# Performance work log

Hardware: AMD Instinct MI355X
Metric: run time of the kernel (lower is better)

## Reference

```python
import jax, jax.numpy as jnp
from jax import lax
import numpy as np

B, C, H, W = 8, 128, 112, 112
G, K, OC = 4, 3, 128
DN = ('NCHW', 'OIHW', 'NCHW')


def setup_inputs() -> dict:
    key = jax.random.key(0)
    k1, k2, k3, k4, k5 = jax.random.split(key, 5)
    x = jax.random.normal(k1, (B, C, H, W), dtype=jnp.float32)
    # kernel_gen: grouped conv, out = K*K*G channels, in/group = C//G
    w_kg = jax.random.normal(k2, (K * K * G, C // G, K, K), dtype=jnp.float32) * 0.05
    b_kg = jax.random.normal(k3, (K * K * G,), dtype=jnp.float32) * 0.05
    # pointwise_conv: grouped 1x1 conv, out = OC, in/group = C//G
    w_pw = jax.random.normal(k4, (OC, C // G, 1, 1), dtype=jnp.float32) * 0.05
    b_pw = jax.random.normal(k5, (OC,), dtype=jnp.float32) * 0.05
    return {"x": x, "w_kg": w_kg, "b_kg": b_kg, "w_pw": w_pw, "b_pw": b_pw}


def reference(x, w_kg, b_kg, w_pw, b_pw):
    b, c, h, w = x.shape
    # dynamic per-pixel kernels: [B, G*K*K, H, W] -> [B, G, K*K, H, W]
    kernel = lax.conv_general_dilated(
        x, w_kg, (1, 1), ((K // 2, K // 2), (K // 2, K // 2)),
        feature_group_count=G, dimension_numbers=DN)
    kernel = kernel + b_kg[None, :, None, None]
    kernel = kernel.reshape(b, G, K * K, h, w)
    # unfold (stride=1, pad=K//2): channel-major, kernel-offset row-major (matches F.unfold)
    p = K // 2
    xp = jnp.pad(x, ((0, 0), (0, 0), (p, p), (p, p)))
    patches = jnp.stack(
        [xp[:, :, i:i + h, j:j + w] for i in range(K) for j in range(K)],
        axis=2)  # [B, C, K*K, H, W]
    patches = patches.reshape(b, G, c // G, K * K, h, w)
    # per-pixel multiply-reduce over kernel taps
    out = (patches * kernel[:, :, None]).sum(axis=3).reshape(b, c, h, w)
    # grouped 1x1 pointwise conv
    out = lax.conv_general_dilated(
        out, w_pw, (1, 1), 'VALID', feature_group_count=G, dimension_numbers=DN)
    return out + b_pw[None, :, None, None]
```

## Files before the change

### kernel.cpp

```cpp
#include <hip/hip_runtime.h>
#include <hip/hip_bf16.h>

typedef __attribute__((ext_vector_type(8))) short short8;
typedef __attribute__((ext_vector_type(4))) float f32x4;
typedef __attribute__((ext_vector_type(4))) unsigned int u32x4;

#define GG 4
#define CC 128
#define HH 112
#define WW 112
#define HWSZ (HH * WW)
#define TH 16
#define TW 16
#define HALO 18
#define NPIX (HALO * HALO)
#define XSTR 32
#define HP 114
#define SLICE_PIX (HP * HP)
#define SLICE_ELE (SLICE_PIX * 32)
#define WK_ELEMS (4 * 9 * 16 * 32)
#define WP_ELEMS (4 * 2 * 16 * 32)
#define W_TOTAL (WK_ELEMS + WP_ELEMS)
#define XT_OFF 32768
#define XT_ELEMS (32 * SLICE_ELE)
#define WS_NEED ((size_t)(XT_OFF + XT_ELEMS) * 2)


__device__ __forceinline__ void reorder_one(int idx,
    const float* __restrict__ w_kg, const float* __restrict__ w_pw,
    unsigned short* __restrict__ ws)
{
    if (idx < WK_ELEMS) {
        int c = idx & 31, t = (idx >> 5) & 15, r = idx >> 9;
        int u = r % 9, g = r / 9;
        float v = (t < 9) ? w_kg[((g * 9 + t) * 32 + c) * 9 + u] : 0.0f;
        ws[idx] = __builtin_bit_cast(unsigned short, __float2bfloat16(v));
    } else if (idx < W_TOTAL) {
        int j = idx - WK_ELEMS;
        int c = j & 31, o = (j >> 5) & 15, mt = (j >> 9) & 1, g = j >> 10;
        float v = w_pw[(g * 32 + mt * 16 + o) * 32 + c];
        ws[idx] = __builtin_bit_cast(unsigned short, __float2bfloat16(v));
    }
}

__global__ __launch_bounds__(256)
void reorder_weights(const float* __restrict__ w_kg, const float* __restrict__ w_pw,
                     unsigned short* __restrict__ ws)
{
    reorder_one(blockIdx.x * 256 + threadIdx.x, w_kg, w_pw, ws);
}

__global__ __launch_bounds__(256, 4)
void transpose_x(const float* __restrict__ x,
                 const float* __restrict__ w_kg, const float* __restrict__ w_pw,
                 unsigned short* __restrict__ ws)
{
    __shared__ unsigned int xsT[16 * 452];
    const int hc = blockIdx.x;
    const int g = blockIdx.y, b = blockIdx.z;
    const int tid = threadIdx.x;
    const int slice = b * GG + g;
    unsigned short* xt = ws + XT_OFF;

    if (hc == 28) {
        #pragma unroll
        for (int k = 0; k < 3; ++k) {
            int off = k * 256 + tid;
            if (off < 704)
                reorder_one(slice * 704 + off, w_kg, w_pw, ws);
        }
        return;
    }
    if (hc == 29) {
        unsigned short* xts = xt + (size_t)slice * SLICE_ELE;
        short8 z = {0, 0, 0, 0, 0, 0, 0, 0};
        #pragma unroll
        for (int k = 0; k < 2; ++k) {
            int i = tid + 256 * k;
            if (i < 452) {
                int pix;
                if (i < 114)      pix = i;
                else if (i < 228) pix = 113 * HP + (i - 114);
                else if (i < 340) pix = (i - 228 + 1) * HP;
                else              pix = (i - 340 + 1) * HP + 113;
                unsigned short* d = xts + (size_t)pix * 32;
                *(short8*)(d)      = z;
                *(short8*)(d + 8)  = z;
                *(short8*)(d + 16) = z;
                *(short8*)(d + 24) = z;
            }
        }
        return;
    }

    const float* xg = x + (size_t)(b * CC + g * 32) * HWSZ + hc * 4 * WW;

    unsigned short* xsT16 = (unsigned short*)xsT;
    #pragma unroll
    for (int k = 0; k < 14; ++k) {
        int t = tid + 256 * k;
        int c = (t * 37450) >> 22;
        int p4 = t - c * 112;
        float4 v = *(const float4*)(xg + (size_t)c * HWSZ + 4 * p4);
        int base = ((c >> 1) * 452 + 4 * p4) * 2 + (c & 1);
        xsT16[base + 0] = __builtin_bit_cast(unsigned short, __float2bfloat16(v.x));
        xsT16[base + 2] = __builtin_bit_cast(unsigned short, __float2bfloat16(v.y));
        xsT16[base + 4] = __builtin_bit_cast(unsigned short, __float2bfloat16(v.z));
        xsT16[base + 6] = __builtin_bit_cast(unsigned short, __float2bfloat16(v.w));
    }
    __syncthreads();

    unsigned short* xts = xt + (size_t)slice * SLICE_ELE;
    #pragma unroll
    for (int k = 0; k < 7; ++k) {
        int t = tid + 256 * k;
        int p = t >> 2, kb = t & 3;
        int row = p / 112;
        int col = p - 112 * row;
        unsigned r[4];
        #pragma unroll
        for (int j = 0; j < 4; ++j)
            r[j] = xsT[(4 * kb + j) * 452 + p];
        size_t pix = (size_t)(hc * 4 + row + 1) * HP + (col + 1);
        *(u32x4*)(xts + pix * 32 + kb * 8) = (u32x4){r[0], r[1], r[2], r[3]};
    }
}

struct Frags {
    short8 afrag[9];
    short8 wpfrag[2];
    float bkv[4];
    float bpv[8];
};

__device__ __forceinline__ void load_frags(Frags& f,
    const unsigned short* __restrict__ wsw,
    const float* __restrict__ b_kg, const float* __restrict__ b_pw,
    int g, int tid)
{
    const int lane = tid & 63;
    const int px   = lane & 15;
    const int kb   = lane >> 4;

    #pragma unroll
    for (int u = 0; u < 9; ++u)
        f.afrag[u] = *(const short8*)(wsw + (((g * 9 + u) * 16 + px) * 32 + kb * 8));
    #pragma unroll
    for (int mt = 0; mt < 2; ++mt)
        f.wpfrag[mt] = *(const short8*)(wsw + WK_ELEMS + (((g * 2 + mt) * 16 + px) * 32 + kb * 8));

    const float* bk = b_kg + g * 9;
    const float* bp = b_pw + g * 32;
    #pragma unroll
    for (int e = 0; e < 4; ++e) {
        int t = 4 * kb + e;
        f.bkv[e] = bk[t < 9 ? t : 0];
    }
    #pragma unroll
    for (int mt = 0; mt < 2; ++mt)
        #pragma unroll
        for (int e = 0; e < 4; ++e)
            f.bpv[mt * 4 + e] = bp[mt * 16 + 4 * kb + e];
}

__device__ __forceinline__ void compute_tile(const Frags& f,
    float* __restrict__ out, unsigned short* xs, float* kvl,
    int g, int b, int h0, int w0, int tid)
{
    const int lane = tid & 63;
    const int wid  = tid >> 6;
    const int px   = lane & 15;
    const int kb   = lane >> 4;

    float* kvp = &kvl[(wid * 16 + px) * 9];
    const size_t obase = ((size_t)(b * CC + g * 32) * HH + h0) * WW + w0 + px;

    #pragma unroll 1
    for (int r = 0; r < 4; ++r) {
        const int py = wid * 4 + r;

        short8 bfrag[9];
        #pragma unroll
        for (int u = 0; u < 9; ++u) {
            int q = (py + u / 3) * HALO + (px + u % 3);
            bfrag[u] = *(const short8*)&xs[q * XSTR + kb * 8];
        }

        f32x4 kv = {0.f, 0.f, 0.f, 0.f};
        #pragma unroll
        for (int u = 0; u < 9; ++u)
            kv = __builtin_amdgcn_mfma_f32_16x16x32_bf16(f.afrag[u], bfrag[u], kv, 0, 0, 0);

        if (kb < 2) {
            #pragma unroll
            for (int i = 0; i < 4; ++i)
                kvp[4 * kb + i] = kv[i] + f.bkv[i];
        } else if (kb == 2) {
            kvp[8] = kv[0] + f.bkv[0];
        }
        float kvv[9];
        #pragma unroll
        for (int t = 0; t < 9; ++t) kvv[t] = kvp[t];

        float m[8] = {0.f, 0.f, 0.f, 0.f, 0.f, 0.f, 0.f, 0.f};
        #pragma unroll
        for (int u = 0; u < 9; ++u) {
            u32x4 bu = __builtin_bit_cast(u32x4, bfrag[u]);
            #pragma unroll
            for (int w = 0; w < 4; ++w) {
                unsigned d = bu[w];
                float lo = __builtin_bit_cast(float, d << 16);
                float hi = __builtin_bit_cast(float, d & 0xffff0000u);
                m[2 * w]     = fmaf(lo, kvv[u], m[2 * w]);
                m[2 * w + 1] = fmaf(hi, kvv[u], m[2 * w + 1]);
            }
        }

        unsigned pk[4];
        #pragma unroll
        for (int w = 0; w < 4; ++w) {
            unsigned slo = __builtin_bit_cast(unsigned short, __float2bfloat16(m[2 * w]));
            unsigned shi = __builtin_bit_cast(unsigned short, __float2bfloat16(m[2 * w + 1]));
            pk[w] = slo | (shi << 16);
        }
        short8 mfrag = __builtin_bit_cast(short8, (u32x4){pk[0], pk[1], pk[2], pk[3]});

        f32x4 zero = {0.f, 0.f, 0.f, 0.f};
        f32x4 o0 = __builtin_amdgcn_mfma_f32_16x16x32_bf16(f.wpfrag[0], mfrag, zero, 0, 0, 0);
        f32x4 o1 = __builtin_amdgcn_mfma_f32_16x16x32_bf16(f.wpfrag[1], mfrag, zero, 0, 0, 0);

        #pragma unroll
        for (int e = 0; e < 4; ++e) {
            int o = 4 * kb + e;
            out[obase + (size_t)o * HWSZ + (size_t)py * WW] = o0[e] + f.bpv[e];
            out[obase + (size_t)(o + 16) * HWSZ + (size_t)py * WW] = o1[e] + f.bpv[4 + e];
        }
    }
}

__global__ __launch_bounds__(256, 4)
void invol_mfma(const unsigned short* __restrict__ ws_all,
                const float* __restrict__ b_kg, const float* __restrict__ b_pw,
                float* __restrict__ out)
{
    __shared__ unsigned short xs[NPIX * XSTR];
    __shared__ float kvl[4 * 16 * 9];

    const int tile  = blockIdx.x;
    const int tileh = tile / 7;
    const int tilew = tile - tileh * 7;
    const int g = blockIdx.y;
    const int b = blockIdx.z;
    const int h0 = tileh * TH;
    const int w0 = tilew * TW;
    const int tid = threadIdx.x;

    {
        const unsigned short* xti = ws_all + XT_OFF + (size_t)(b * GG + g) * SLICE_ELE;
        #pragma unroll
        for (int k = 0; k < 6; ++k) {
            int t = tid + 256 * k;
            if (t < 1296) {
                int q = t >> 2, kb2 = t & 3;
                int r = (q * 57) >> 10;
                int col = q - 18 * r;
                const unsigned short* src =
                    xti + ((size_t)((h0 + r) * HP + (w0 + col)) * 32 + kb2 * 8);
                __builtin_amdgcn_global_load_lds(src, &xs[t * 8], 16, 0, 0);
            }
        }
    }

    Frags f;
    load_frags(f, ws_all, b_kg, b_pw, g, tid);

    __syncthreads();

    compute_tile(f, out, xs, kvl, g, b, h0, w0, tid);
}

__global__ __launch_bounds__(256, 4)
void invol_mfma_fb(const float* __restrict__ x,
                   const float* __restrict__ b_kg, const float* __restrict__ b_pw,
                   const unsigned short* __restrict__ ws, float* __restrict__ out)
{
    __shared__ unsigned short xs[NPIX * XSTR];
    __shared__ float kvl[4 * 16 * 9];

    const int tile  = blockIdx.x;
    const int tileh = tile / 7;
    const int tilew = tile - tileh * 7;
    const int g = blockIdx.y;
    const int b = blockIdx.z;
    const int h0 = tileh * TH;
    const int w0 = tilew * TW;
    const int tid = threadIdx.x;

    Frags f;
    load_frags(f, ws, b_kg, b_pw, g, tid);

    {
        const float* xg = x + (size_t)(b * CC + g * 32) * HWSZ;
        int c = 0, q = tid;
        #pragma unroll
        for (int batch = 0; batch < 3; ++batch) {
            const int bn = (batch == 2) ? 13 : 14;
            float v[14];
            int pki[14];
            #pragma unroll
            for (int it = 0; it < bn; ++it) {
                const int itg = batch * 14 + it;
                const bool valid = (itg < 40) || (tid < 128);
                int r   = (q * 57) >> 10;
                int col = q - 18 * r;
                int gh = h0 - 1 + r;
                int gw = w0 - 1 + col;
                bool ok = valid && ((unsigned)gh < (unsigned)HH) && ((unsigned)gw < (unsigned)WW);
                int ghc = min(max(gh, 0), HH - 1);
                int gwc = min(max(gw, 0), WW - 1);
                int cc  = min(c, 31);
                float t = xg[(size_t)cc * HWSZ + ghc * WW + gwc];
                v[it]   = ok ? t : 0.0f;
                pki[it] = (c < 32) ? (q * XSTR + c) : 0;
                q += 256; if (q >= NPIX) { q -= NPIX; ++c; }
            }
            #pragma unroll
            for (int it = 0; it < bn; ++it) {
                unsigned short val = __builtin_bit_cast(unsigned short, __float2bfloat16(v[it]));
                if (pki[it] || it == 0) xs[pki[it]] = val;
            }
        }
    }
    __syncthreads();

    compute_tile(f, out, xs, kvl, g, b, h0, w0, tid);
}

extern "C" void kernel_launch(void* const* d_in, const int* in_sizes, int n_in,
                              void* d_out, int out_size, void* d_ws, size_t ws_size,
                              hipStream_t stream)
{
    const float* x    = (const float*)d_in[0];
    const float* w_kg = (const float*)d_in[1];
    const float* b_kg = (const float*)d_in[2];
    const float* w_pw = (const float*)d_in[3];
    const float* b_pw = (const float*)d_in[4];
    float* out = (float*)d_out;
    unsigned short* ws = (unsigned short*)d_ws;

    if (ws_size >= WS_NEED) {
        hipLaunchKernelGGL(transpose_x, dim3(30, GG, 8), dim3(256), 0, stream,
                           x, w_kg, w_pw, ws);
        hipLaunchKernelGGL(invol_mfma, dim3(49, GG, 8), dim3(256), 0, stream,
                           ws, b_kg, b_pw, out);
    } else {
        int pre_blocks = (W_TOTAL + 255) / 256;
        hipLaunchKernelGGL(reorder_weights, dim3(pre_blocks), dim3(256), 0, stream,
                           w_kg, w_pw, ws);
        hipLaunchKernelGGL(invol_mfma_fb, dim3(49, GG, 8), dim3(256), 0, stream,
                           x, b_kg, b_pw, ws, out);
    }
}
```

Measured before the change: 36.00 us.

## Give each wave a private halo slice in LDS and drop block barrier

Each wave now loads its own 6-row halo strip (4 output rows plus 2 halo rows) into a private LDS region. That replaces the shared 18x18 tile and the block-wide __syncthreads with a per-wave vmcnt wait. The goal is to remove inter-wave synchronisation so waves start computing as soon as their own data arrives. In exchange, halo rows are loaded redundantly (24 rows instead of 18) and the LDS footprint grows, which could reduce occupancy. The per-wave kvl use already appears wave-private.

```diff
diff --git a/kernel.cpp b/kernel.cpp
--- a/kernel.cpp
+++ b/kernel.cpp
@@ -15,6 +15,8 @@
 #define HALO 18
 #define NPIX (HALO * HALO)
 #define XSTR 32
+#define WCH 432
+#define WUS (WCH * 8)
 #define HP 114
 #define SLICE_PIX (HP * HP)
 #define SLICE_ELE (SLICE_PIX * 32)
@@ -163,6 +165,7 @@
             f.bpv[mt * 4 + e] = bp[mt * 16 + 4 * kb + e];
 }
 
+template<bool WL>
 __device__ __forceinline__ void compute_tile(const Frags& f,
     float* __restrict__ out, unsigned short* xs, float* kvl,
     int g, int b, int h0, int w0, int tid)
@@ -172,6 +175,7 @@
     const int px   = lane & 15;
     const int kb   = lane >> 4;
 
+    const unsigned short* xw = WL ? (xs + wid * WUS) : xs;
     float* kvp = &kvl[(wid * 16 + px) * 9];
     const size_t obase = ((size_t)(b * CC + g * 32) * HH + h0) * WW + w0 + px;
 
@@ -182,8 +186,9 @@
         short8 bfrag[9];
         #pragma unroll
         for (int u = 0; u < 9; ++u) {
-            int q = (py + u / 3) * HALO + (px + u % 3);
-            bfrag[u] = *(const short8*)&xs[q * XSTR + kb * 8];
+            int prow = WL ? (r + u / 3) : (py + u / 3);
+            int pix  = prow * HALO + (px + u % 3);
+            bfrag[u] = *(const short8*)&xw[pix * XSTR + kb * 8];
         }
 
         f32x4 kv = {0.f, 0.f, 0.f, 0.f};
@@ -243,7 +248,7 @@
                 const float* __restrict__ b_kg, const float* __restrict__ b_pw,
                 float* __restrict__ out)
 {
-    __shared__ unsigned short xs[NPIX * XSTR];
+    __shared__ unsigned short xs[4 * WUS];
     __shared__ float kvl[4 * 16 * 9];
 
     const int tile  = blockIdx.x;
@@ -254,19 +259,23 @@
     const int h0 = tileh * TH;
     const int w0 = tilew * TW;
     const int tid = threadIdx.x;
+    const int lane = tid & 63;
+    const int wid  = tid >> 6;
 
     {
         const unsigned short* xti = ws_all + XT_OFF + (size_t)(b * GG + g) * SLICE_ELE;
-        #pragma unroll
-        for (int k = 0; k < 6; ++k) {
-            int t = tid + 256 * k;
-            if (t < 1296) {
-                int q = t >> 2, kb2 = t & 3;
-                int r = (q * 57) >> 10;
-                int col = q - 18 * r;
+        const int R0 = wid * 4;
+        unsigned short* xw = xs + wid * WUS;
+        #pragma unroll
+        for (int k = 0; k < 7; ++k) {
+            int t = lane + 64 * k;
+            if (k < 6 || t < WCH) {
+                int lr  = (t * 57) >> 12;
+                int rem = t - 72 * lr;
+                int col = rem >> 2, kb2 = rem & 3;
                 const unsigned short* src =
-                    xti + ((size_t)((h0 + r) * HP + (w0 + col)) * 32 + kb2 * 8);
-                __builtin_amdgcn_global_load_lds(src, &xs[t * 8], 16, 0, 0);
+                    xti + ((size_t)((h0 + R0 + lr) * HP + (w0 + col)) * 32 + kb2 * 8);
+                __builtin_amdgcn_global_load_lds(src, &xw[t * 8], 16, 0, 0);
             }
         }
     }
@@ -274,9 +283,10 @@
     Frags f;
     load_frags(f, ws_all, b_kg, b_pw, g, tid);
 
-    __syncthreads();
-
-    compute_tile(f, out, xs, kvl, g, b, h0, w0, tid);
+    asm volatile("s_waitcnt vmcnt(0)" ::: "memory");
+    __builtin_amdgcn_sched_barrier(0);
+
+    compute_tile<true>(f, out, xs, kvl, g, b, h0, w0, tid);
 }
 
 __global__ __launch_bounds__(256, 4)
@@ -333,7 +343,7 @@
     }
     __syncthreads();
 
-    compute_tile(f, out, xs, kvl, g, b, h0, w0, tid);
+    compute_tile<false>(f, out, xs, kvl, g, b, h0, w0, tid);
 }
 
 extern "C" void kernel_launch(void* const* d_in, const int* in_sizes, int n_in,
```

Measured after the change: 35.98 us. No clear change (-0.0%).
